# Optimization experiments

Hardware: AMD Instinct MI355X
Metric: run time of the kernel (lower is better)

## Reference

```python
import jax, jax.numpy as jnp
import numpy as np

B, C, H, W, K = 4, 64, 128, 128, 3
K2 = K * K
PAD = (K - 1) // 2  # same padding for 3x3


def setup_inputs() -> dict:
    key = jax.random.key(0)
    ks = jax.random.split(key, 9)
    s = 0.05
    return {
        "x": jax.random.normal(ks[0], (B, C, H, W), jnp.float32),
        "inter": jax.random.normal(ks[1], (B, C, H, W), jnp.float32),
        # offset/mask predictor conv: input cat([x, inter]) -> 3*K2 channels (dy, dx, mask)
        "w_offset": jax.random.normal(ks[2], (3 * K2, 2 * C, K, K), jnp.float32) * s,
        "b_offset": jnp.zeros((3 * K2,), jnp.float32),
        # deformable conv weight (bias=False per DGM init)
        "w_dcn": jax.random.normal(ks[3], (C, C, K, K), jnp.float32) * s,
        # SFT gamma branch: two 1x1 convs (bias=False)
        "w_g1": jax.random.normal(ks[4], (C, C), jnp.float32) * s,
        "w_g2": jax.random.normal(ks[5], (C, C), jnp.float32) * s,
        # SFT beta branch: two 1x1 convs (bias=False)
        "w_b1": jax.random.normal(ks[6], (C, C), jnp.float32) * s,
        "w_b2": jax.random.normal(ks[7], (C, C), jnp.float32) * s,
    }


def _lrelu(v):
    # LeakyReLU(0.1)
    return jnp.where(v >= 0, v, 0.1 * v)


def _conv(x, w, b=None):
    y = jax.lax.conv_general_dilated(
        x, w, window_strides=(1, 1), padding=[(PAD, PAD), (PAD, PAD)],
        dimension_numbers=("NCHW", "OIHW", "NCHW"))
    if b is not None:
        y = y + b[None, :, None, None]
    return y


def _bilinear_gather(x, py, px):
    """x: [B,C,H,W]; py, px: [B,K2,H,W] float sample coords.
    Returns samples [B,K2,H,W,C]; out-of-bounds treated as zero (DCN zero-pad)."""
    y0 = jnp.floor(py)
    x0 = jnp.floor(px)
    wy = (py - y0)[..., None]
    wx = (px - x0)[..., None]

    def gather(yi, xi):
        valid = ((yi >= 0) & (yi < H) & (xi >= 0) & (xi < W)).astype(x.dtype)
        yc = jnp.clip(yi, 0, H - 1).astype(jnp.int32)
        xc = jnp.clip(xi, 0, W - 1).astype(jnp.int32)
        bidx = jnp.arange(B)[:, None, None, None]
        v = x[bidx, :, yc, xc]  # advanced indexing -> [B,K2,H,W,C]
        return v * valid[..., None]

    v00 = gather(y0, x0)
    v01 = gather(y0, x0 + 1)
    v10 = gather(y0 + 1, x0)
    v11 = gather(y0 + 1, x0 + 1)
    return (v00 * (1 - wy) * (1 - wx) + v01 * (1 - wy) * wx
            + v10 * wy * (1 - wx) + v11 * wy * wx)


def _dgm_forward(x, inter, w_offset, b_offset, w_dcn, w_g1, w_g2, w_b1, w_b2):
    # --- WADCN branch: modulated deformable conv, offsets predicted from cat(x, inter)
    om = _conv(jnp.concatenate([x, inter], axis=1), w_offset, b_offset)  # [B,3K2,H,W]
    dy, dx, m = jnp.split(om, 3, axis=1)  # each [B,K2,H,W]
    mask = jax.nn.sigmoid(m)

    ky, kx = jnp.meshgrid(jnp.arange(K), jnp.arange(K), indexing="ij")
    ky = ky.reshape(K2).astype(x.dtype)
    kx = kx.reshape(K2).astype(x.dtype)
    hh = jnp.arange(H, dtype=x.dtype)
    ww = jnp.arange(W, dtype=x.dtype)
    # sample coords: base grid + kernel-tap offset + learned offset
    py = hh[None, None, :, None] + (ky - PAD)[None, :, None, None] + dy  # [B,K2,H,W]
    px = ww[None, None, None, :] + (kx - PAD)[None, :, None, None] + dx

    samp = _bilinear_gather(x, py, px) * mask[..., None]  # [B,K2,H,W,C]
    dcn_out = jnp.einsum("bkhwc,ock->bohw", samp, w_dcn.reshape(C, C, K2))

    # --- SFT branch: two 1x1-conv + LeakyReLU chains producing gamma/beta
    gamma = jnp.einsum("oc,bchw->bohw", w_g2,
                       _lrelu(jnp.einsum("oc,bchw->bohw", w_g1, inter)))
    beta = jnp.einsum("oc,bchw->bohw", w_b2,
                      _lrelu(jnp.einsum("oc,bchw->bohw", w_b1, inter)))
    sft_out = x * gamma + beta

    # --- fused residual combine (DGM.relu is defined but never applied)
    return x + dcn_out + sft_out


def reference(x, inter, w_offset, b_offset, w_dcn, w_g1, w_g2, w_b1, w_b2):
    return _dgm_forward(x, inter, w_offset, b_offset, w_dcn, w_g1, w_g2, w_b1, w_b2)
```

## Files before the change

### kernel.cpp

```cpp
#include <hip/hip_runtime.h>
#include <hip/hip_bf16.h>
#include <math.h>

#define BB 4
#define CC 64
#define HH 128
#define WW 128
#define HW (HH*WW)
#define NPIX (BB*HW)

typedef __attribute__((ext_vector_type(8))) short short8;
typedef __attribute__((ext_vector_type(4))) float f32x4;

__device__ __forceinline__ float bf2f(ushort u) {
  union { unsigned u; float f; } v; v.u = ((unsigned)u) << 16; return v.f;
}
__device__ __forceinline__ ushort f2bf(float f) {
  __hip_bfloat16 h = __float2bfloat16(f); return *(ushort*)&h;
}

__global__ __launch_bounds__(256) void k_prep(
    const float* __restrict__ x, const float* __restrict__ inter,
    const float* __restrict__ w_off, const float* __restrict__ w_dcn,
    const float* __restrict__ wg1, const float* __restrict__ wb1,
    const float* __restrict__ wg2, const float* __restrict__ wb2,
    ushort* __restrict__ x_clh, ushort* __restrict__ inter_clh,
    ushort* __restrict__ wfb, ushort* __restrict__ wdT,
    ushort* __restrict__ w1gb, ushort* __restrict__ w1bb,
    ushort* __restrict__ w2gb, ushort* __restrict__ w2bb,
    float* __restrict__ zp) {
  __shared__ __align__(16) float tile[64 * 128];
  int blk = blockIdx.x;
  int tid = threadIdx.x;
  if (blk < 1024) {
    int sel = blk >> 9;
    int bh = blk & 511;
    int b = bh >> 7, h = bh & 127;
    const float* src = sel ? inter : x;
    ushort* dst = sel ? inter_clh : x_clh;
    const float* sp = src + (size_t)(b * 64) * HW + h * WW;
#pragma unroll
    for (int it = 0; it < 8; ++it) {
      int idx = it * 256 + tid;
      int c = idx >> 5, wq = idx & 31;
      float4 v = *(const float4*)(sp + (size_t)c * HW + wq * 4);
      int s = (c >> 3) & 7;
      *(float4*)(&tile[c * 128 + ((wq ^ s) << 2)]) = v;
    }
    __syncthreads();
    ushort* dp = dst + ((size_t)b * HW + h * WW) * 64;
#pragma unroll
    for (int it = 0; it < 4; ++it) {
      int idx = it * 256 + tid;
      int w = idx >> 3, c8 = idx & 7;
      short8 outv;
#pragma unroll
      for (int j = 0; j < 8; ++j) {
        int c = c8 * 8 + j;
        int sl = (w >> 2) ^ c8;
        float f = tile[c * 128 + (sl << 2) + (w & 3)];
        outv[j] = (short)f2bf(f);
      }
      *(short8*)(dp + (size_t)w * 64 + c8 * 8) = outv;
    }
  } else if (blk < 1168) {
    int i = (blk - 1024) * 256 + tid;
    if (i < 64) zp[i] = 0.f;
    if (i < 9 * 32 * 128) {
      int tap = i >> 12, rem = i & 4095, m = rem >> 7, c = rem & 127;
      float v = (m < 27) ? w_off[(size_t)(m * 128 + c) * 9 + tap] : 0.f;
      wfb[i] = f2bf(v);
    }
  } else if (blk < 1312) {
    int i = (blk - 1168) * 256 + tid;
    if (i < 64 * 64 * 9) {
      int o = i / 576, rem = i % 576, k = rem >> 6, c = rem & 63;
      wdT[i] = f2bf(w_dcn[(o * 64 + c) * 9 + k]);
    }
  } else {
    int i = (blk - 1312) * 256 + tid;
    int m = i >> 12, j = i & 4095;
    const float* src = (m == 0) ? wg1 : (m == 1) ? wb1 : (m == 2) ? wg2 : wb2;
    ushort* dst = (m == 0) ? w1gb : (m == 1) ? w1bb : (m == 2) ? w2gb : w2bb;
    dst[j] = f2bf(src[j]);
  }
}

#define NPX 64
#define FPX 72
#define SP2 584

__global__ __launch_bounds__(256) void k_omega(
    const float* __restrict__ x, const ushort* __restrict__ x_clh,
    const ushort* __restrict__ inter_clh,
    const float* __restrict__ b_off, const ushort* __restrict__ wfb,
    const ushort* __restrict__ wdT,
    const ushort* __restrict__ w1gb, const ushort* __restrict__ w1bb,
    const ushort* __restrict__ w2gb, const ushort* __restrict__ w2bb,
    const ushort* __restrict__ zp16, float* __restrict__ out) {
  __shared__ __align__(16) ushort LDSB[24448];
  ushort* halo = LDSB;
  ushort* Sg = LDSB;
  ushort* Sb = LDSB + 4608;
  float* oml = (float*)(LDSB + 9216);
  int*   cy  = (int*)LDSB;
  int*   cx  = cy + 576;
  float* cwy = (float*)(cx + 576);
  float* cwx = cwy + 576;
  float* cm  = cwx + 576;
  ushort* S  = LDSB + 5760;

  int tid = threadIdx.x;
  int wave = tid >> 6, lane = tid & 63;
  int quad = lane >> 4, col = lane & 15;
  int g = tid & 7;
  int bid = blockIdx.x;
  int wid = (bid & 7) * 128 + (bid >> 3);
  int pg0 = wid * NPX;
  int b = pg0 >> 14, hw0 = pg0 & 16383;
  int h = hw0 >> 7, w0 = hw0 & 127;
  int pt = wave >> 1, mt = wave & 1;
  int o_base = __builtin_amdgcn_readfirstlane(wave * 16);

  f32x4 accx[2], acci[2];
  {
    int ch = (tid & 7) * 8;
    unsigned bbase = (unsigned)b * HW;
    const ushort* wb0 = wfb + (size_t)(mt * 16 + col) * 128 + quad * 8;
#pragma unroll 1
    for (int pass = 0; pass < 2; ++pass) {
      const ushort* sb = pass ? inter_clh : x_clh;
#pragma unroll
      for (int it = 0; it < 7; ++it) {
        int e = it * 32 + (tid >> 3);
        if (e < 198) {
          int row = e / 66, pxl = e % 66;
          int hs = h + row - 1;
          int ps = w0 + pxl - 1;
          bool ok = ((unsigned)hs < 128u) && ((unsigned)ps < 128u);
          int hc = hs < 0 ? 0 : (hs > 127 ? 127 : hs);
          int pc = ps < 0 ? 0 : (ps > 127 ? 127 : ps);
          short8 v = *(const short8*)(sb + ((size_t)(bbase + (hc << 7) + pc)) * 64 + ch);
          short8 z = {0, 0, 0, 0, 0, 0, 0, 0};
          if (!ok) v = z;
          *(short8*)(&halo[e * 72 + ch]) = v;
        }
      }
      __syncthreads();
      int aoff = pass ? 64 : 0;
      f32x4 ap0 = {0.f, 0.f, 0.f, 0.f}, ap1 = {0.f, 0.f, 0.f, 0.f};
#pragma unroll
      for (int ky = 0; ky < 3; ++ky) {
#pragma unroll
        for (int kx = 0; kx < 3; ++kx) {
          const ushort* wt = wb0 + (size_t)(ky * 3 + kx) * 4096 + aoff;
#pragma unroll
          for (int ks = 0; ks < 2; ++ks) {
            short8 a = *(const short8*)(wt + ks * 32);
            short8 b0 = *(const short8*)(&halo[(ky * 66 + pt * 32 + col + kx) * 72 + ks * 32 + quad * 8]);
            ap0 = __builtin_amdgcn_mfma_f32_16x16x32_bf16(a, b0, ap0, 0, 0, 0);
            short8 b1 = *(const short8*)(&halo[(ky * 66 + pt * 32 + 16 + col + kx) * 72 + ks * 32 + quad * 8]);
            ap1 = __builtin_amdgcn_mfma_f32_16x16x32_bf16(a, b1, ap1, 0, 0, 0);
          }
        }
      }
      if (pass) { acci[0] = ap0; acci[1] = ap1; }
      else      { accx[0] = ap0; accx[1] = ap1; }
      __syncthreads();
    }
  }

#pragma unroll
  for (int nt2 = 0; nt2 < 2; ++nt2)
#pragma unroll
    for (int r = 0; r < 4; ++r) {
      int o = mt * 16 + quad * 4 + r;
      if (o < 27) oml[o * 66 + pt * 32 + nt2 * 16 + col] = accx[nt2][r] + acci[nt2][r];
    }

  f32x4 ag[4], ab[4];
#pragma unroll
  for (int nt = 0; nt < 4; ++nt) {
    ag[nt] = (f32x4){0.f, 0.f, 0.f, 0.f};
    ab[nt] = (f32x4){0.f, 0.f, 0.f, 0.f};
  }
#pragma unroll
  for (int ks = 0; ks < 2; ++ks) {
    short8 a_g = *(const short8*)(w1gb + (size_t)(o_base + col) * 64 + ks * 32 + quad * 8);
    short8 a_b = *(const short8*)(w1bb + (size_t)(o_base + col) * 64 + ks * 32 + quad * 8);
#pragma unroll
    for (int nt = 0; nt < 4; ++nt) {
      short8 bf = *(const short8*)(inter_clh + (size_t)(pg0 + nt * 16 + col) * 64 + ks * 32 + quad * 8);
      ag[nt] = __builtin_amdgcn_mfma_f32_16x16x32_bf16(a_g, bf, ag[nt], 0, 0, 0);
      ab[nt] = __builtin_amdgcn_mfma_f32_16x16x32_bf16(a_b, bf, ab[nt], 0, 0, 0);
    }
  }
#pragma unroll
  for (int nt = 0; nt < 4; ++nt) {
    int px = nt * 16 + col;
    ushort pkg[4], pkb[4];
#pragma unroll
    for (int r = 0; r < 4; ++r) {
      float vg = ag[nt][r]; vg = vg >= 0.f ? vg : 0.1f * vg;
      float vb = ab[nt][r]; vb = vb >= 0.f ? vb : 0.1f * vb;
      pkg[r] = f2bf(vg); pkb[r] = f2bf(vb);
    }
    *(uint2*)(&Sg[px * FPX + o_base + quad * 4]) = *(uint2*)pkg;
    *(uint2*)(&Sb[px * FPX + o_base + quad * 4]) = *(uint2*)pkb;
  }
  __syncthreads();

  f32x4 gg[4], gb[4];
#pragma unroll
  for (int nt = 0; nt < 4; ++nt) {
    gg[nt] = (f32x4){0.f, 0.f, 0.f, 0.f};
    gb[nt] = (f32x4){0.f, 0.f, 0.f, 0.f};
  }
#pragma unroll
  for (int ks = 0; ks < 2; ++ks) {
    short8 a_g = *(const short8*)(w2gb + (size_t)(o_base + col) * 64 + ks * 32 + quad * 8);
    short8 a_b = *(const short8*)(w2bb + (size_t)(o_base + col) * 64 + ks * 32 + quad * 8);
#pragma unroll
    for (int nt = 0; nt < 4; ++nt) {
      short8 bgf = *(const short8*)(Sg + (nt * 16 + col) * FPX + ks * 32 + quad * 8);
      short8 bbf = *(const short8*)(Sb + (nt * 16 + col) * FPX + ks * 32 + quad * 8);
      gg[nt] = __builtin_amdgcn_mfma_f32_16x16x32_bf16(a_g, bgf, gg[nt], 0, 0, 0);
      gb[nt] = __builtin_amdgcn_mfma_f32_16x16x32_bf16(a_b, bbf, gb[nt], 0, 0, 0);
    }
  }
  float ev[4][4];
#pragma unroll
  for (int nt = 0; nt < 4; ++nt)
#pragma unroll
    for (int r = 0; r < 4; ++r) {
      int o = o_base + quad * 4 + r;
      float xv = x[(size_t)(b * 64 + o) * HW + hw0 + nt * 16 + col];
      ev[nt][r] = xv + xv * gg[nt][r] + gb[nt][r];
    }
  __syncthreads();

  for (int i = tid; i < 9 * NPX; i += 256) {
    int t = i >> 6, p = i & 63;
    float dy = oml[t * 66 + p] + b_off[t];
    float dx = oml[(9 + t) * 66 + p] + b_off[9 + t];
    float mz = oml[(18 + t) * 66 + p] + b_off[18 + t];
    float py = (float)(h + (t / 3) - 1) + dy;
    float px = (float)(w0 + p + (t % 3) - 1) + dx;
    float y0f = floorf(py), x0f = floorf(px);
    cy[i] = (int)y0f;
    cx[i] = (int)x0f;
    cwy[i] = py - y0f;
    cwx[i] = px - x0f;
    cm[i] = 1.f / (1.f + __expf(-mz));
  }
  __syncthreads();

  f32x4 acc[4];
#pragma unroll
  for (int nt = 0; nt < 4; ++nt) acc[nt] = (f32x4){0.f, 0.f, 0.f, 0.f};

  const ushort* bp = x_clh + (size_t)b * HW * 64;
  int p = tid >> 3;

#pragma unroll 1
  for (int half = 0; half < 2; ++half) {
    if (half) __syncthreads();
#pragma unroll 3
    for (int t = 0; t < 9; ++t) {
      int idx = t * 64 + half * 32 + p;
      int y0 = cy[idx], x0 = cx[idx];
      float wy = cwy[idx], wx = cwx[idx], m = cm[idx];
      bool yok0 = (unsigned)y0 < 128u, yok1 = (unsigned)(y0 + 1) < 128u;
      bool xok0 = (unsigned)x0 < 128u, xok1 = (unsigned)(x0 + 1) < 128u;
      const ushort* r0 = bp + ((size_t)(int)((y0 << 7) + x0)) * 64 + g * 8;
      const ushort* r1 = r0 + (size_t)WW * 64;
      short8 s00 = *(const short8*)((yok0 && xok0) ? r0 : zp16);
      short8 s01 = *(const short8*)((yok0 && xok1) ? (r0 + 64) : zp16);
      short8 s10 = *(const short8*)((yok1 && xok0) ? r1 : zp16);
      short8 s11 = *(const short8*)((yok1 && xok1) ? (r1 + 64) : zp16);
      short8 outv;
#pragma unroll
      for (int j = 0; j < 8; ++j) {
        float v00 = bf2f((ushort)s00[j]), v01 = bf2f((ushort)s01[j]);
        float v10 = bf2f((ushort)s10[j]), v11 = bf2f((ushort)s11[j]);
        float top = v00 + (v01 - v00) * wx;
        float bot = v10 + (v11 - v10) * wx;
        float val = top + (bot - top) * wy;
        outv[j] = (short)f2bf(val * m);
      }
      *(short8*)(&S[p * SP2 + t * 64 + g * 8]) = outv;
    }
    __syncthreads();
    const ushort* wrow = wdT + (size_t)(o_base + col) * 576 + quad * 8;
    const ushort* srow = S + quad * 8;
#pragma unroll
    for (int ks = 0; ks < 18; ++ks) {
      short8 a = *(const short8*)(wrow + ks * 32);
#pragma unroll
      for (int ntl = 0; ntl < 2; ++ntl) {
        short8 bfv = *(const short8*)(srow + (ntl * 16 + col) * SP2 + ks * 32);
        acc[half * 2 + ntl] = __builtin_amdgcn_mfma_f32_16x16x32_bf16(a, bfv, acc[half * 2 + ntl], 0, 0, 0);
      }
    }
  }

#pragma unroll
  for (int nt = 0; nt < 4; ++nt)
#pragma unroll
    for (int r = 0; r < 4; ++r) {
      int o = o_base + quad * 4 + r;
      size_t idx = (size_t)(b * 64 + o) * HW + hw0 + nt * 16 + col;
      out[idx] = ev[nt][r] + acc[nt][r];
    }
}

extern "C" void kernel_launch(void* const* d_in, const int* in_sizes, int n_in,
                              void* d_out, int out_size, void* d_ws, size_t ws_size,
                              hipStream_t stream) {
  const float* x     = (const float*)d_in[0];
  const float* inter = (const float*)d_in[1];
  const float* w_off = (const float*)d_in[2];
  const float* b_off = (const float*)d_in[3];
  const float* w_dcn = (const float*)d_in[4];
  const float* wg1   = (const float*)d_in[5];
  const float* wg2   = (const float*)d_in[6];
  const float* wb1   = (const float*)d_in[7];
  const float* wb2   = (const float*)d_in[8];
  float* out = (float*)d_out;

  float* ws        = (float*)d_ws;
  ushort* x_clh    = (ushort*)ws;
  ushort* inter_clh= (ushort*)(ws + 2097152);
  ushort* wfb      = (ushort*)(ws + 4194304);
  ushort* wdT      = (ushort*)(ws + 4212736);
  ushort* w1gb     = (ushort*)(ws + 4231168);
  ushort* w1bb     = (ushort*)(ws + 4233216);
  ushort* w2gb     = (ushort*)(ws + 4235264);
  ushort* w2bb     = (ushort*)(ws + 4237312);
  float* zp        = ws + 4239360;

  k_prep<<<1376, 256, 0, stream>>>(x, inter, w_off, w_dcn, wg1, wb1, wg2, wb2,
                                   x_clh, inter_clh, wfb, wdT,
                                   w1gb, w1bb, w2gb, w2bb, zp);

  k_omega<<<1024, 256, 0, stream>>>(x, x_clh, inter_clh, b_off, wfb, wdT,
                                    w1gb, w1bb, w2gb, w2bb,
                                    (const ushort*)zp, out);
}
```

Before: 166.9 us.

## Double k_omega block to 512 threads and split pixel tiles across waves

Raises the fused DGM kernel from 256 to 512 threads per block. The 8 waves now split the offset conv, SFT and DCN MFMA work by pixel half and output-channel group, each holding fewer accumulators. The bilinear gather is reassigned so all 512 threads share the 9x32x8 sample work. The aim is more waves per CU for latency hiding and less serial gather work per thread. The cost is more threads contending for LDS and barriers, and duplicated weight fragment loads across the pixel-half waves.

```diff
diff --git a/kernel.cpp b/kernel.cpp
--- a/kernel.cpp
+++ b/kernel.cpp
@@ -90,7 +90,7 @@
 #define FPX 72
 #define SP2 584
 
-__global__ __launch_bounds__(256) void k_omega(
+__global__ __launch_bounds__(512) void k_omega(
     const float* __restrict__ x, const ushort* __restrict__ x_clh,
     const ushort* __restrict__ inter_clh,
     const float* __restrict__ b_off, const ushort* __restrict__ wfb,
@@ -113,26 +113,27 @@
   int tid = threadIdx.x;
   int wave = tid >> 6, lane = tid & 63;
   int quad = lane >> 4, col = lane & 15;
-  int g = tid & 7;
   int bid = blockIdx.x;
   int wid = (bid & 7) * 128 + (bid >> 3);
   int pg0 = wid * NPX;
   int b = pg0 >> 14, hw0 = pg0 & 16383;
   int h = hw0 >> 7, w0 = hw0 & 127;
   int pt = wave >> 1, mt = wave & 1;
-  int o_base = __builtin_amdgcn_readfirstlane(wave * 16);
-
-  f32x4 accx[2], acci[2];
+  int ph = wave >> 2, og = wave & 3;
+  int o_base = __builtin_amdgcn_readfirstlane(og * 16);
+
+  f32x4 accx = {0.f, 0.f, 0.f, 0.f}, acci = {0.f, 0.f, 0.f, 0.f};
   {
     int ch = (tid & 7) * 8;
     unsigned bbase = (unsigned)b * HW;
     const ushort* wb0 = wfb + (size_t)(mt * 16 + col) * 128 + quad * 8;
+    int pxb = pt * 16 + col;
 #pragma unroll 1
     for (int pass = 0; pass < 2; ++pass) {
       const ushort* sb = pass ? inter_clh : x_clh;
 #pragma unroll
-      for (int it = 0; it < 7; ++it) {
-        int e = it * 32 + (tid >> 3);
+      for (int it = 0; it < 4; ++it) {
+        int e = it * 64 + (tid >> 3);
         if (e < 198) {
           int row = e / 66, pxl = e % 66;
           int hs = h + row - 1;
@@ -148,7 +149,7 @@
       }
       __syncthreads();
       int aoff = pass ? 64 : 0;
-      f32x4 ap0 = {0.f, 0.f, 0.f, 0.f}, ap1 = {0.f, 0.f, 0.f, 0.f};
+      f32x4 ap = {0.f, 0.f, 0.f, 0.f};
 #pragma unroll
       for (int ky = 0; ky < 3; ++ky) {
 #pragma unroll
@@ -157,30 +158,25 @@
 #pragma unroll
           for (int ks = 0; ks < 2; ++ks) {
             short8 a = *(const short8*)(wt + ks * 32);
-            short8 b0 = *(const short8*)(&halo[(ky * 66 + pt * 32 + col + kx) * 72 + ks * 32 + quad * 8]);
-            ap0 = __builtin_amdgcn_mfma_f32_16x16x32_bf16(a, b0, ap0, 0, 0, 0);
-            short8 b1 = *(const short8*)(&halo[(ky * 66 + pt * 32 + 16 + col + kx) * 72 + ks * 32 + quad * 8]);
-            ap1 = __builtin_amdgcn_mfma_f32_16x16x32_bf16(a, b1, ap1, 0, 0, 0);
+            short8 bv = *(const short8*)(&halo[(ky * 66 + pxb + kx) * 72 + ks * 32 + quad * 8]);
+            ap = __builtin_amdgcn_mfma_f32_16x16x32_bf16(a, bv, ap, 0, 0, 0);
           }
         }
       }
-      if (pass) { acci[0] = ap0; acci[1] = ap1; }
-      else      { accx[0] = ap0; accx[1] = ap1; }
+      if (pass) acci = ap; else accx = ap;
       __syncthreads();
     }
   }
 
 #pragma unroll
-  for (int nt2 = 0; nt2 < 2; ++nt2)
-#pragma unroll
-    for (int r = 0; r < 4; ++r) {
-      int o = mt * 16 + quad * 4 + r;
-      if (o < 27) oml[o * 66 + pt * 32 + nt2 * 16 + col] = accx[nt2][r] + acci[nt2][r];
-    }
-
-  f32x4 ag[4], ab[4];
-#pragma unroll
-  for (int nt = 0; nt < 4; ++nt) {
+  for (int r = 0; r < 4; ++r) {
+    int o = mt * 16 + quad * 4 + r;
+    if (o < 27) oml[o * 66 + pt * 16 + col] = accx[r] + acci[r];
+  }
+
+  f32x4 ag[2], ab[2];
+#pragma unroll
+  for (int nt = 0; nt < 2; ++nt) {
     ag[nt] = (f32x4){0.f, 0.f, 0.f, 0.f};
     ab[nt] = (f32x4){0.f, 0.f, 0.f, 0.f};
   }
@@ -189,15 +185,15 @@
     short8 a_g = *(const short8*)(w1gb + (size_t)(o_base + col) * 64 + ks * 32 + quad * 8);
     short8 a_b = *(const short8*)(w1bb + (size_t)(o_base + col) * 64 + ks * 32 + quad * 8);
 #pragma unroll
-    for (int nt = 0; nt < 4; ++nt) {
-      short8 bf = *(const short8*)(inter_clh + (size_t)(pg0 + nt * 16 + col) * 64 + ks * 32 + quad * 8);
+    for (int nt = 0; nt < 2; ++nt) {
+      short8 bf = *(const short8*)(inter_clh + (size_t)(pg0 + ph * 32 + nt * 16 + col) * 64 + ks * 32 + quad * 8);
       ag[nt] = __builtin_amdgcn_mfma_f32_16x16x32_bf16(a_g, bf, ag[nt], 0, 0, 0);
       ab[nt] = __builtin_amdgcn_mfma_f32_16x16x32_bf16(a_b, bf, ab[nt], 0, 0, 0);
     }
   }
 #pragma unroll
-  for (int nt = 0; nt < 4; ++nt) {
-    int px = nt * 16 + col;
+  for (int nt = 0; nt < 2; ++nt) {
+    int px = ph * 32 + nt * 16 + col;
     ushort pkg[4], pkb[4];
 #pragma unroll
     for (int r = 0; r < 4; ++r) {
@@ -210,36 +206,38 @@
   }
   __syncthreads();
 
-  f32x4 gg[4], gb[4];
-#pragma unroll
-  for (int nt = 0; nt < 4; ++nt) {
-    gg[nt] = (f32x4){0.f, 0.f, 0.f, 0.f};
-    gb[nt] = (f32x4){0.f, 0.f, 0.f, 0.f};
+  f32x4 gg[2], gb[2];
+#pragma unroll
+  for (int hh = 0; hh < 2; ++hh) {
+    gg[hh] = (f32x4){0.f, 0.f, 0.f, 0.f};
+    gb[hh] = (f32x4){0.f, 0.f, 0.f, 0.f};
   }
 #pragma unroll
   for (int ks = 0; ks < 2; ++ks) {
     short8 a_g = *(const short8*)(w2gb + (size_t)(o_base + col) * 64 + ks * 32 + quad * 8);
     short8 a_b = *(const short8*)(w2bb + (size_t)(o_base + col) * 64 + ks * 32 + quad * 8);
 #pragma unroll
-    for (int nt = 0; nt < 4; ++nt) {
-      short8 bgf = *(const short8*)(Sg + (nt * 16 + col) * FPX + ks * 32 + quad * 8);
-      short8 bbf = *(const short8*)(Sb + (nt * 16 + col) * FPX + ks * 32 + quad * 8);
-      gg[nt] = __builtin_amdgcn_mfma_f32_16x16x32_bf16(a_g, bgf, gg[nt], 0, 0, 0);
-      gb[nt] = __builtin_amdgcn_mfma_f32_16x16x32_bf16(a_b, bbf, gb[nt], 0, 0, 0);
-    }
-  }
-  float ev[4][4];
-#pragma unroll
-  for (int nt = 0; nt < 4; ++nt)
+    for (int hh = 0; hh < 2; ++hh) {
+      int px = hh * 32 + ph * 16 + col;
+      short8 bgf = *(const short8*)(Sg + (size_t)px * FPX + ks * 32 + quad * 8);
+      short8 bbf = *(const short8*)(Sb + (size_t)px * FPX + ks * 32 + quad * 8);
+      gg[hh] = __builtin_amdgcn_mfma_f32_16x16x32_bf16(a_g, bgf, gg[hh], 0, 0, 0);
+      gb[hh] = __builtin_amdgcn_mfma_f32_16x16x32_bf16(a_b, bbf, gb[hh], 0, 0, 0);
+    }
+  }
+  float ev[2][4];
+#pragma unroll
+  for (int hh = 0; hh < 2; ++hh)
 #pragma unroll
     for (int r = 0; r < 4; ++r) {
       int o = o_base + quad * 4 + r;
-      float xv = x[(size_t)(b * 64 + o) * HW + hw0 + nt * 16 + col];
-      ev[nt][r] = xv + xv * gg[nt][r] + gb[nt][r];
+      int px = hh * 32 + ph * 16 + col;
+      float xv = x[(size_t)(b * 64 + o) * HW + hw0 + px];
+      ev[hh][r] = xv + xv * gg[hh][r] + gb[hh][r];
     }
   __syncthreads();
 
-  for (int i = tid; i < 9 * NPX; i += 256) {
+  for (int i = tid; i < 9 * NPX; i += 512) {
     int t = i >> 6, p = i & 63;
     float dy = oml[t * 66 + p] + b_off[t];
     float dx = oml[(9 + t) * 66 + p] + b_off[9 + t];
@@ -255,62 +253,64 @@
   }
   __syncthreads();
 
-  f32x4 acc[4];
-#pragma unroll
-  for (int nt = 0; nt < 4; ++nt) acc[nt] = (f32x4){0.f, 0.f, 0.f, 0.f};
+  f32x4 acc[2];
+  acc[0] = (f32x4){0.f, 0.f, 0.f, 0.f};
+  acc[1] = (f32x4){0.f, 0.f, 0.f, 0.f};
 
   const ushort* bp = x_clh + (size_t)b * HW * 64;
-  int p = tid >> 3;
 
 #pragma unroll 1
   for (int half = 0; half < 2; ++half) {
     if (half) __syncthreads();
-#pragma unroll 3
-    for (int t = 0; t < 9; ++t) {
-      int idx = t * 64 + half * 32 + p;
-      int y0 = cy[idx], x0 = cx[idx];
-      float wy = cwy[idx], wx = cwx[idx], m = cm[idx];
-      bool yok0 = (unsigned)y0 < 128u, yok1 = (unsigned)(y0 + 1) < 128u;
-      bool xok0 = (unsigned)x0 < 128u, xok1 = (unsigned)(x0 + 1) < 128u;
-      const ushort* r0 = bp + ((size_t)(int)((y0 << 7) + x0)) * 64 + g * 8;
-      const ushort* r1 = r0 + (size_t)WW * 64;
-      short8 s00 = *(const short8*)((yok0 && xok0) ? r0 : zp16);
-      short8 s01 = *(const short8*)((yok0 && xok1) ? (r0 + 64) : zp16);
-      short8 s10 = *(const short8*)((yok1 && xok0) ? r1 : zp16);
-      short8 s11 = *(const short8*)((yok1 && xok1) ? (r1 + 64) : zp16);
-      short8 outv;
-#pragma unroll
-      for (int j = 0; j < 8; ++j) {
-        float v00 = bf2f((ushort)s00[j]), v01 = bf2f((ushort)s01[j]);
-        float v10 = bf2f((ushort)s10[j]), v11 = bf2f((ushort)s11[j]);
-        float top = v00 + (v01 - v00) * wx;
-        float bot = v10 + (v11 - v10) * wx;
-        float val = top + (bot - top) * wy;
-        outv[j] = (short)f2bf(val * m);
+#pragma unroll 1
+    for (int it = 0; it < 5; ++it) {
+      int tau = it * 512 + tid;
+      if (tau < 2304) {
+        int tp = tau >> 3, g8 = tau & 7;
+        int t = tp >> 5, p = tp & 31;
+        int idx = t * 64 + half * 32 + p;
+        int y0 = cy[idx], x0 = cx[idx];
+        float wy = cwy[idx], wx = cwx[idx], m = cm[idx];
+        bool yok0 = (unsigned)y0 < 128u, yok1 = (unsigned)(y0 + 1) < 128u;
+        bool xok0 = (unsigned)x0 < 128u, xok1 = (unsigned)(x0 + 1) < 128u;
+        const ushort* r0 = bp + ((size_t)(int)((y0 << 7) + x0)) * 64 + g8 * 8;
+        const ushort* r1 = r0 + (size_t)WW * 64;
+        short8 s00 = *(const short8*)((yok0 && xok0) ? r0 : (zp16 + g8 * 8));
+        short8 s01 = *(const short8*)((yok0 && xok1) ? (r0 + 64) : (zp16 + g8 * 8));
+        short8 s10 = *(const short8*)((yok1 && xok0) ? r1 : (zp16 + g8 * 8));
+        short8 s11 = *(const short8*)((yok1 && xok1) ? (r1 + 64) : (zp16 + g8 * 8));
+        short8 outv;
+#pragma unroll
+        for (int j = 0; j < 8; ++j) {
+          float v00 = bf2f((ushort)s00[j]), v01 = bf2f((ushort)s01[j]);
+          float v10 = bf2f((ushort)s10[j]), v11 = bf2f((ushort)s11[j]);
+          float top = v00 + (v01 - v00) * wx;
+          float bot = v10 + (v11 - v10) * wx;
+          float val = top + (bot - top) * wy;
+          outv[j] = (short)f2bf(val * m);
+        }
+        *(short8*)(&S[p * SP2 + t * 64 + g8 * 8]) = outv;
       }
-      *(short8*)(&S[p * SP2 + t * 64 + g * 8]) = outv;
     }
     __syncthreads();
     const ushort* wrow = wdT + (size_t)(o_base + col) * 576 + quad * 8;
-    const ushort* srow = S + quad * 8;
+    const ushort* srow = S + (size_t)(ph * 16 + col) * SP2 + quad * 8;
 #pragma unroll
     for (int ks = 0; ks < 18; ++ks) {
       short8 a = *(const short8*)(wrow + ks * 32);
-#pragma unroll
-      for (int ntl = 0; ntl < 2; ++ntl) {
-        short8 bfv = *(const short8*)(srow + (ntl * 16 + col) * SP2 + ks * 32);
-        acc[half * 2 + ntl] = __builtin_amdgcn_mfma_f32_16x16x32_bf16(a, bfv, acc[half * 2 + ntl], 0, 0, 0);
-      }
-    }
-  }
-
-#pragma unroll
-  for (int nt = 0; nt < 4; ++nt)
+      short8 bfv = *(const short8*)(srow + ks * 32);
+      acc[half] = __builtin_amdgcn_mfma_f32_16x16x32_bf16(a, bfv, acc[half], 0, 0, 0);
+    }
+  }
+
+#pragma unroll
+  for (int hh = 0; hh < 2; ++hh)
 #pragma unroll
     for (int r = 0; r < 4; ++r) {
       int o = o_base + quad * 4 + r;
-      size_t idx = (size_t)(b * 64 + o) * HW + hw0 + nt * 16 + col;
-      out[idx] = ev[nt][r] + acc[nt][r];
+      int px = hh * 32 + ph * 16 + col;
+      size_t idx = (size_t)(b * 64 + o) * HW + hw0 + px;
+      out[idx] = ev[hh][r] + acc[hh][r];
     }
 }
 
@@ -343,7 +343,7 @@
                                    x_clh, inter_clh, wfb, wdT,
                                    w1gb, w1bb, w2gb, w2bb, zp);
 
-  k_omega<<<1024, 256, 0, stream>>>(x, x_clh, inter_clh, b_off, wfb, wdT,
+  k_omega<<<1024, 512, 0, stream>>>(x, x_clh, inter_clh, b_off, wfb, wdT,
                                     w1gb, w1bb, w2gb, w2bb,
                                     (const ushort*)zp, out);
 }
```

Result: slower. 220.2 us (+31.9%).
